# Kernel optimization log

Hardware: AMD Instinct MI355X
Metric: run time of the kernel (lower is better)

The kernel has to match this reference:

```python
import jax, jax.numpy as jnp
import numpy as np

B, S, D = 8, 512, 768
HEADS = 16           # label_n
HD = 64              # size_per_head
NEG = 1e12


def setup_inputs() -> dict:
    key = jax.random.key(0)
    k1, k2, k3 = jax.random.split(key, 3)
    hidden = jax.random.normal(k1, (B, S, D), dtype=jnp.float32)
    token_ids = jax.random.randint(k2, (B, S), 0, 21128, dtype=jnp.int32)
    W = jax.random.normal(k3, (D, HEADS * 2 * HD), dtype=jnp.float32) * 0.02
    b = jnp.zeros((HEADS * 2 * HD,), dtype=jnp.float32)
    return {"hidden": hidden, "token_ids": token_ids, "W": W, "b": b}


def _rope(x):
    # x: [B, S, H, HD] -> RoPE-rotated, Su Jianlin interleaved convention
    d = x.shape[-1]
    inv_freq = 1.0 / (10000.0 ** (jnp.arange(0, d, 2, dtype=jnp.float32) / d))  # [d/2]
    pos = jnp.arange(x.shape[1], dtype=jnp.float32)                              # [S]
    freqs = pos[:, None] * inv_freq[None, :]                                     # [S, d/2]
    sin = jnp.repeat(jnp.sin(freqs), 2, axis=-1)[None, :, None, :]               # [1,S,1,d]
    cos = jnp.repeat(jnp.cos(freqs), 2, axis=-1)[None, :, None, :]
    x2 = jnp.stack([-x[..., 1::2], x[..., 0::2]], axis=-1).reshape(x.shape)
    return x * cos + x2 * sin


def reference(hidden, token_ids, W, b):
    # qk projection: [B,S,H,2,HD]
    qk = (hidden @ W + b).reshape(B, S, HEADS, 2, HD)
    q, k = qk[..., 0, :], qk[..., 1, :]          # [B,S,H,HD]
    q = _rope(q)
    k = _rope(k)
    # all-pairs span scores per entity head
    logits = jnp.einsum('bmhd,bnhd->bhmn', q, k) / jnp.sqrt(jnp.float32(HD))
    # padding mask from token ids (0 = pad)
    mask = (token_ids > 0).astype(logits.dtype)  # [B,S]
    logits = logits - (1.0 - mask[:, None, :, None]) * NEG
    logits = logits - (1.0 - mask[:, None, None, :]) * NEG
    # strict lower-triangular mask (spans must have start <= end)
    tril = jnp.tril(jnp.ones((S, S), dtype=logits.dtype), k=-1)
    logits = logits - tril[None, None, :, :] * NEG
    # valid-span weight mask (upper triangle incl. diag, both positions valid)
    tri_mask = (1.0 - tril)[None, None, :, :] * mask[:, None, :, None] * mask[:, None, None, :]
    return logits, tri_mask
```

## Files before the change

kernel.cpp:

```cpp
#include <hip/hip_runtime.h>
#include <hip/hip_bf16.h>
#include <cstdint>
#include <cstddef>


#define NEGV 1.0e12f

typedef short bf16x8 __attribute__((ext_vector_type(8)));
typedef float f32x4  __attribute__((ext_vector_type(4)));
typedef char  char16v __attribute__((ext_vector_type(16)));

static __device__ __forceinline__ short f2b(float x) {
    __hip_bfloat16 h = __float2bfloat16(x);
    union { __hip_bfloat16 h; short s; } u; u.h = h; return u.s;
}
static __device__ __forceinline__ void gload16(const void* g, void* l) {
    __builtin_amdgcn_global_load_lds(
        (const __attribute__((address_space(1))) void*)g,
        (__attribute__((address_space(3))) void*)l, 16, 0, 0);
}

__global__ __launch_bounds__(256) void prep_kernel(const float* __restrict__ hidden,
                                                   const float* __restrict__ W,
                                                   char* __restrict__ Xf,
                                                   char* __restrict__ Wt,
                                                   float* __restrict__ SinT,
                                                   float* __restrict__ CosT) {
    __shared__ char T[64 * 68];
    int blk = blockIdx.x, tid = threadIdx.x;
    if (blk < 1536) {
        int t = blk * 256 + tid;
        const float4* hp = (const float4*)hidden;
        float4 a = hp[t * 2], c = hp[t * 2 + 1];
        int lo = __builtin_amdgcn_cvt_pk_fp8_f32(a.x, a.y, 0, false);
        lo     = __builtin_amdgcn_cvt_pk_fp8_f32(a.z, a.w, lo, true);
        int hi = __builtin_amdgcn_cvt_pk_fp8_f32(c.x, c.y, 0, false);
        hi     = __builtin_amdgcn_cvt_pk_fp8_f32(c.z, c.w, hi, true);
        int2 o; o.x = lo; o.y = hi;
        *(int2*)(Xf + (size_t)t * 8) = o;
    } else if (blk < 1600) {
        int u = (blk - 1536) * 256 + tid;
        int s = u >> 5, i = u & 31;
        float ang = (float)s * exp2f(-0.4152410118609203f * (float)i);
        float sn, cs; __sincosf(ang, &sn, &cs);
        SinT[u] = sn; CosT[u] = cs;
    } else {
        int tb = blk - 1600;
        int k0 = (tb % 12) * 64, n0 = (tb / 12) * 64;
        int r = tid >> 2, cb = (tid & 3) * 4;
#pragma unroll
        for (int q = 0; q < 4; ++q) {
            int c = cb + q * 16;
            float4 v = *(const float4*)(W + (size_t)(k0 + r) * 2048 + n0 + c);
            int p = __builtin_amdgcn_cvt_pk_fp8_f32(v.x * 16.f, v.y * 16.f, 0, false);
            p     = __builtin_amdgcn_cvt_pk_fp8_f32(v.z * 16.f, v.w * 16.f, p, true);
            *(int*)(T + r * 68 + c) = p;
        }
        __syncthreads();
        int n = tid >> 2, kc = (tid & 3) * 16;
        char16v o;
#pragma unroll
        for (int j = 0; j < 16; ++j)
            o[j] = T[(kc + j) * 68 + n];
        *(char16v*)(Wt + (size_t)(n0 + n) * 768 + k0 + kc) = o;
    }
}

__global__ __launch_bounds__(256) void gemm_rope(const char* __restrict__ A,
                                                 const char* __restrict__ Bt,
                                                 const float* __restrict__ bias,
                                                 const float* __restrict__ SinT,
                                                 const float* __restrict__ CosT,
                                                 short* __restrict__ Qb,
                                                 short* __restrict__ Kb) {
    __shared__ char As[128 * 64];
    __shared__ char Bs[128 * 64];
    const int m0 = (blockIdx.x >> 4) * 128;
    const int n0 = (blockIdx.x & 15) * 128;
    const int tid  = threadIdx.x;
    const int wave = tid >> 6, lane = tid & 63;
    const int quad = lane >> 4, r16 = lane & 15;
    const int wm = (wave >> 1) * 64, wn = (wave & 1) * 64;

    const int lr  = lane >> 2;
    const int gcc = ((lane & 3) ^ (lr & 3)) * 16;
    const int r0  = wave * 32 + lr;
    const char* gA0 = A  + (size_t)(m0 + r0) * 768 + gcc;
    const char* gA1 = A  + (size_t)(m0 + r0 + 16) * 768 + gcc;
    const char* gB0 = Bt + (size_t)(n0 + r0) * 768 + gcc;
    const char* gB1 = Bt + (size_t)(n0 + r0 + 16) * 768 + gcc;
    char* lA0 = As + (wave * 32) * 64;
    char* lA1 = As + (wave * 32 + 16) * 64;
    char* lB0 = Bs + (wave * 32) * 64;
    char* lB1 = Bs + (wave * 32 + 16) * 64;

    const int swk = r16 & 3;
    const int in8 = (quad & 1) * 8;

    f32x4 acc[4][4] = {};
    for (int k0 = 0; k0 < 768; k0 += 64) {
        __syncthreads();
        gload16(gA0 + k0, lA0);
        gload16(gA1 + k0, lA1);
        gload16(gB0 + k0, lB0);
        gload16(gB1 + k0, lB1);
        __syncthreads();

#pragma unroll
        for (int kb = 0; kb < 2; ++kb) {
            const int chunk = ((kb * 2 + (quad >> 1)) ^ swk) * 16 + in8;
            long af[4], bfr[4];
#pragma unroll
            for (int mi = 0; mi < 4; ++mi)
                af[mi] = *(const long*)(As + (wm + mi * 16 + r16) * 64 + chunk);
#pragma unroll
            for (int ni = 0; ni < 4; ++ni)
                bfr[ni] = *(const long*)(Bs + (wn + ni * 16 + r16) * 64 + chunk);
#pragma unroll
            for (int mi = 0; mi < 4; ++mi)
#pragma unroll
                for (int ni = 0; ni < 4; ++ni)
                    acc[mi][ni] = __builtin_amdgcn_mfma_f32_16x16x32_fp8_fp8(
                        af[mi], bfr[ni], acc[mi][ni], 0, 0, 0);
        }
    }

    const int b     = m0 >> 9;
    const int s0l   = (m0 & 511) + wm + quad * 4;
    const int h     = n0 >> 7;
    const int which = wn >> 6;
    short* dstT = (which ? Kb : Qb) + (size_t)(b * 16 + h) * 512 * 64;
    const float sgn = (r16 & 1) ? 1.0f : -1.0f;
#pragma unroll
    for (int ni = 0; ni < 4; ++ni) {
        int col = n0 + wn + ni * 16 + r16;
        float bv = bias[col];
        int d  = ni * 16 + r16;
        int ii = d >> 1;
#pragma unroll
        for (int mi = 0; mi < 4; ++mi)
#pragma unroll
            for (int r = 0; r < 4; ++r) {
                int s = s0l + mi * 16 + r;
                float v  = acc[mi][ni][r] * 0.0625f + bv;
                float pv = __shfl_xor(v, 1);
                float sn = SinT[s * 32 + ii];
                float cs = CosT[s * 32 + ii];
                dstT[(size_t)s * 64 + d] = f2b(v * cs + sgn * pv * sn);
            }
    }
}

__global__ __launch_bounds__(256) void logits_kernel(const short* __restrict__ Qb,
                                                     const short* __restrict__ Kb,
                                                     const int* __restrict__ tok,
                                                     float* __restrict__ out,
                                                     float* __restrict__ out2) {
    __shared__ short Qs[128 * 64];
    __shared__ short Ks[128 * 64];
    __shared__ float rowNeg[128];
    __shared__ float colNeg[128];

    int blk = blockIdx.x;
    int nt = blk & 3, mt = (blk >> 2) & 3, bh = blk >> 4;
    int b = bh >> 4, h = bh & 15;
    int m0 = mt * 128, n0 = nt * 128;

    const int tid  = threadIdx.x;
    const int wave = tid >> 6, lane = tid & 63;
    const int quad = lane >> 4, r16 = lane & 15;
    const int wm = (wave >> 1) * 64, wn = (wave & 1) * 64;

    const short* gsrc = (wave < 2)
        ? Qb + ((size_t)bh * 512 + m0) * 64
        : Kb + ((size_t)bh * 512 + n0) * 64;
    short* ldst = (wave < 2) ? Qs : Ks;
    const int wv = wave & 1;
    const int gc = ((lane & 7) ^ (lane >> 3)) * 8;
    const int rl = wv * 64 + (lane >> 3);
#pragma unroll
    for (int j = 0; j < 8; ++j)
        gload16(gsrc + (rl + j * 8) * 64 + gc, ldst + wv * 4096 + j * 512);

    if (tid < 128)      rowNeg[tid]       = (tok[b * 512 + m0 + tid] > 0) ? 0.f : NEGV;
    else if (tid < 256) colNeg[tid - 128] = (tok[b * 512 + n0 + (tid - 128)] > 0) ? 0.f : NEGV;
    __syncthreads();

    const int sw8 = r16 & 7;
    f32x4 acc[4][4] = {};
#pragma unroll
    for (int kb = 0; kb < 2; ++kb) {
        bf16x8 af[4], bfr[4];
#pragma unroll
        for (int mi = 0; mi < 4; ++mi)
            af[mi] = *(const bf16x8*)(Qs + (wm + mi * 16 + r16) * 64
                                         + ((quad + kb * 4) ^ sw8) * 8);
#pragma unroll
        for (int ni = 0; ni < 4; ++ni)
            bfr[ni] = *(const bf16x8*)(Ks + (wn + ni * 16 + r16) * 64
                                          + ((quad + kb * 4) ^ sw8) * 8);
#pragma unroll
        for (int mi = 0; mi < 4; ++mi)
#pragma unroll
            for (int ni = 0; ni < 4; ++ni)
                acc[mi][ni] = __builtin_amdgcn_mfma_f32_16x16x32_bf16(
                    af[mi], bfr[ni], acc[mi][ni], 0, 0, 0);
    }

    float* obase = out + (size_t)bh * 512 * 512;
#pragma unroll
    for (int mi = 0; mi < 4; ++mi)
#pragma unroll
        for (int ni = 0; ni < 4; ++ni) {
            int n = n0 + wn + ni * 16 + r16;
            float cn = colNeg[n - n0];
#pragma unroll
            for (int r = 0; r < 4; ++r) {
                int m = m0 + wm + mi * 16 + quad * 4 + r;
                float v = acc[mi][ni][r] * 0.125f - rowNeg[m - m0] - cn
                          - ((m > n) ? NEGV : 0.0f);
                obase[(size_t)m * 512 + n] = v;
            }
        }

    if (h == 0) {
        float* o2 = out2 + (size_t)b * 262144;
#pragma unroll
        for (int mi = 0; mi < 4; ++mi)
#pragma unroll
            for (int ni = 0; ni < 4; ++ni) {
                int n = n0 + wn + ni * 16 + r16;
                float mn = (colNeg[n - n0] == 0.f) ? 1.f : 0.f;
#pragma unroll
                for (int r = 0; r < 4; ++r) {
                    int m = m0 + wm + mi * 16 + quad * 4 + r;
                    float mm = (rowNeg[m - m0] == 0.f) ? 1.f : 0.f;
                    o2[(size_t)m * 512 + n] = (m > n) ? 0.f : (mm * mn);
                }
            }
    }
}

extern "C" void kernel_launch(void* const* d_in, const int* in_sizes, int n_in,
                              void* d_out, int out_size, void* d_ws, size_t ws_size,
                              hipStream_t stream) {
    const float* hidden = (const float*)d_in[0];
    const int*   tok    = (const int*)d_in[1];
    const float* W      = (const float*)d_in[2];
    const float* bias   = (const float*)d_in[3];
    float* out  = (float*)d_out;
    float* out2 = out + 33554432;

    char* ws = (char*)d_ws;
    char*  Xf   = (char*)(ws);
    char*  Wt   = (char*)(ws + 3145728);
    float* SinT = (float*)(ws + 4718592);
    float* CosT = (float*)(ws + 4784128);
    short* Qb   = (short*)(ws + 4849664);
    short* Kb   = (short*)(ws + 13238272);

    hipLaunchKernelGGL(prep_kernel,   dim3(1984), dim3(256), 0, stream,
                       hidden, W, Xf, Wt, SinT, CosT);
    hipLaunchKernelGGL(gemm_rope,     dim3(512),  dim3(256), 0, stream,
                       Xf, Wt, bias, SinT, CosT, Qb, Kb);
    hipLaunchKernelGGL(logits_kernel, dim3(2048), dim3(256), 0, stream,
                       Qb, Kb, tok, out, out2);
}
```

Measured before the change: 189.2 us.

## Swap MFMA operand order for row-contiguous accumulators and vectorized stores

Both GEMM kernels now pass B as the first MFMA operand and A as the second, so each lane's four accumulator values lie along the output column. That lets the projection epilogue apply RoPE within a lane, with no shuffle, and write 4-wide bf16 vectors. It also lets the logits kernel emit 16-byte nontemporal float4 stores in place of scattered scalar stores. The 1/sqrt(HD) scale is folded into the Q projection (vscale/bscale), which removes the multiply from the logits epilogue but rounds a pre-scaled Q to bf16.

```diff
diff --git a/kernel.cpp b/kernel.cpp
--- a/kernel.cpp
+++ b/kernel.cpp
@@ -8,6 +8,7 @@
 
 typedef short bf16x8 __attribute__((ext_vector_type(8)));
 typedef float f32x4  __attribute__((ext_vector_type(4)));
+typedef short sh4    __attribute__((ext_vector_type(4)));
 typedef char  char16v __attribute__((ext_vector_type(16)));
 
 static __device__ __forceinline__ short f2b(float x) {
@@ -117,37 +118,43 @@
             for (int ni = 0; ni < 4; ++ni)
                 bfr[ni] = *(const long*)(Bs + (wn + ni * 16 + r16) * 64 + chunk);
 #pragma unroll
-            for (int mi = 0; mi < 4; ++mi)
-#pragma unroll
-                for (int ni = 0; ni < 4; ++ni)
-                    acc[mi][ni] = __builtin_amdgcn_mfma_f32_16x16x32_fp8_fp8(
-                        af[mi], bfr[ni], acc[mi][ni], 0, 0, 0);
+            for (int ni = 0; ni < 4; ++ni)
+#pragma unroll
+                for (int mi = 0; mi < 4; ++mi)
+                    acc[ni][mi] = __builtin_amdgcn_mfma_f32_16x16x32_fp8_fp8(
+                        bfr[ni], af[mi], acc[ni][mi], 0, 0, 0);
         }
     }
 
     const int b     = m0 >> 9;
-    const int s0l   = (m0 & 511) + wm + quad * 4;
     const int h     = n0 >> 7;
     const int which = wn >> 6;
     short* dstT = (which ? Kb : Qb) + (size_t)(b * 16 + h) * 512 * 64;
-    const float sgn = (r16 & 1) ? 1.0f : -1.0f;
+    const float vscale = which ? 0.0625f : 0.0078125f;
+    const float bscale = which ? 1.0f : 0.125f;
 #pragma unroll
     for (int ni = 0; ni < 4; ++ni) {
-        int col = n0 + wn + ni * 16 + r16;
-        float bv = bias[col];
-        int d  = ni * 16 + r16;
-        int ii = d >> 1;
-#pragma unroll
-        for (int mi = 0; mi < 4; ++mi)
-#pragma unroll
-            for (int r = 0; r < 4; ++r) {
-                int s = s0l + mi * 16 + r;
-                float v  = acc[mi][ni][r] * 0.0625f + bv;
-                float pv = __shfl_xor(v, 1);
-                float sn = SinT[s * 32 + ii];
-                float cs = CosT[s * 32 + ii];
-                dstT[(size_t)s * 64 + d] = f2b(v * cs + sgn * pv * sn);
-            }
+        const int db = ni * 16 + quad * 4;
+        f32x4 bv = *(const f32x4*)(bias + n0 + wn + db);
+        const int ii = db >> 1;
+#pragma unroll
+        for (int mi = 0; mi < 4; ++mi) {
+            const int s = (m0 & 511) + wm + mi * 16 + r16;
+            const float* Ct = CosT + s * 32 + ii;
+            const float* St = SinT + s * 32 + ii;
+            float c0 = Ct[0], sn0 = St[0], c1 = Ct[1], sn1 = St[1];
+            f32x4 a = acc[ni][mi];
+            float v0 = a[0] * vscale + bv[0] * bscale;
+            float v1 = a[1] * vscale + bv[1] * bscale;
+            float v2 = a[2] * vscale + bv[2] * bscale;
+            float v3 = a[3] * vscale + bv[3] * bscale;
+            sh4 o;
+            o[0] = f2b(v0 * c0 - v1 * sn0);
+            o[1] = f2b(v1 * c0 + v0 * sn0);
+            o[2] = f2b(v2 * c1 - v3 * sn1);
+            o[3] = f2b(v3 * c1 + v2 * sn1);
+            *(sh4*)(dstT + (size_t)s * 64 + db) = o;
+        }
     }
 }
 
@@ -187,7 +194,7 @@
     __syncthreads();
 
     const int sw8 = r16 & 7;
-    f32x4 acc[4][4] = {};
+    f32x4 a2[4][4] = {};
 #pragma unroll
     for (int kb = 0; kb < 2; ++kb) {
         bf16x8 af[4], bfr[4];
@@ -200,44 +207,55 @@
             bfr[ni] = *(const bf16x8*)(Ks + (wn + ni * 16 + r16) * 64
                                           + ((quad + kb * 4) ^ sw8) * 8);
 #pragma unroll
-        for (int mi = 0; mi < 4; ++mi)
-#pragma unroll
-            for (int ni = 0; ni < 4; ++ni)
-                acc[mi][ni] = __builtin_amdgcn_mfma_f32_16x16x32_bf16(
-                    af[mi], bfr[ni], acc[mi][ni], 0, 0, 0);
-    }
-
-    float* obase = out + (size_t)bh * 512 * 512;
-#pragma unroll
-    for (int mi = 0; mi < 4; ++mi)
-#pragma unroll
-        for (int ni = 0; ni < 4; ++ni) {
-            int n = n0 + wn + ni * 16 + r16;
-            float cn = colNeg[n - n0];
+        for (int ni = 0; ni < 4; ++ni)
+#pragma unroll
+            for (int mi = 0; mi < 4; ++mi)
+                a2[ni][mi] = __builtin_amdgcn_mfma_f32_16x16x32_bf16(
+                    bfr[ni], af[mi], a2[ni][mi], 0, 0, 0);
+    }
+
+    float* obase = out + (size_t)bh * 262144;
+    float rn[4];
+#pragma unroll
+    for (int mi = 0; mi < 4; ++mi) rn[mi] = rowNeg[wm + mi * 16 + r16];
+#pragma unroll
+    for (int ni = 0; ni < 4; ++ni) {
+        int nb = wn + ni * 16 + quad * 4;
+        f32x4 cn4 = *(const f32x4*)(colNeg + nb);
+        int gn = n0 + nb;
+#pragma unroll
+        for (int mi = 0; mi < 4; ++mi) {
+            int gm = m0 + wm + mi * 16 + r16;
+            f32x4 a = a2[ni][mi], v;
 #pragma unroll
             for (int r = 0; r < 4; ++r) {
-                int m = m0 + wm + mi * 16 + quad * 4 + r;
-                float v = acc[mi][ni][r] * 0.125f - rowNeg[m - m0] - cn
-                          - ((m > n) ? NEGV : 0.0f);
-                obase[(size_t)m * 512 + n] = v;
+                float x = a[r] - rn[mi] - cn4[r];
+                v[r] = (gm > gn + r) ? x - NEGV : x;
             }
-        }
+            __builtin_nontemporal_store(v, (f32x4*)(obase + (size_t)gm * 512 + gn));
+        }
+    }
 
     if (h == 0) {
         float* o2 = out2 + (size_t)b * 262144;
 #pragma unroll
-        for (int mi = 0; mi < 4; ++mi)
+        for (int mi = 0; mi < 4; ++mi) {
+            int ml = wm + mi * 16 + r16;
+            int gm = m0 + ml;
+            float mm = (rowNeg[ml] == 0.f) ? 1.f : 0.f;
 #pragma unroll
             for (int ni = 0; ni < 4; ++ni) {
-                int n = n0 + wn + ni * 16 + r16;
-                float mn = (colNeg[n - n0] == 0.f) ? 1.f : 0.f;
+                int nb = wn + ni * 16 + quad * 4;
+                int gn = n0 + nb;
+                f32x4 v;
 #pragma unroll
                 for (int r = 0; r < 4; ++r) {
-                    int m = m0 + wm + mi * 16 + quad * 4 + r;
-                    float mm = (rowNeg[m - m0] == 0.f) ? 1.f : 0.f;
-                    o2[(size_t)m * 512 + n] = (m > n) ? 0.f : (mm * mn);
+                    float mn = (colNeg[nb + r] == 0.f) ? 1.f : 0.f;
+                    v[r] = (gm > gn + r) ? 0.f : (mm * mn);
                 }
+                __builtin_nontemporal_store(v, (f32x4*)(o2 + (size_t)gm * 512 + gn));
             }
+        }
     }
 }
 
```

Measured after the change: 202.3 us. 1.07x slower.
